# Optimization experiments

Measured on AMD Instinct MI355X. Metric: run time of the kernel, lower is better.

## Reference

```python
import jax, jax.numpy as jnp
import numpy as np

N_NODES = 100000
N_EDGES = 1200000
N_GRAPHS = 2048
NUM_SHAPE, NUM_COLOR, NUM_CLASS = 8, 8, 10
MAX_POS, EMB, HID = 20, 16, 64
IN_DIM = 3 * EMB  # 48


def setup_inputs() -> dict:
    key = jax.random.key(0)
    ks = jax.random.split(key, 14)
    x = jax.random.randint(ks[0], (N_NODES, 3), 0, NUM_SHAPE)
    edge_index = jax.random.randint(ks[1], (2, N_EDGES), 0, N_NODES)
    batch = jnp.sort(jax.random.randint(ks[2], (N_NODES,), 0, N_GRAPHS))
    s = 0.1
    return {
        'x': x, 'edge_index': edge_index, 'batch': batch, 'num_graphs': N_GRAPHS,
        'shape_emb': jax.random.normal(ks[3], (NUM_SHAPE, EMB)) * s,
        'color_emb': jax.random.normal(ks[4], (NUM_COLOR, EMB)) * s,
        'pos_emb': jax.random.normal(ks[5], (MAX_POS, EMB)) * s,
        'W1_l': jax.random.normal(ks[6], (IN_DIM, HID)) * s,
        'W1_r': jax.random.normal(ks[7], (IN_DIM, HID)) * s,
        'b1': jnp.zeros((HID,)),
        'W2_l': jax.random.normal(ks[8], (HID, HID)) * s,
        'W2_r': jax.random.normal(ks[9], (HID, HID)) * s,
        'b2': jnp.zeros((HID,)),
        'Wc': jax.random.normal(ks[10], (HID, NUM_CLASS)) * s,
        'bc': jnp.zeros((NUM_CLASS,)),
    }


def _sage(h, src, dst, W_l, W_r, b, n_nodes):
    # mean-aggregate neighbor features x[src] into dst, then linear combine with root
    agg = jax.ops.segment_sum(h[src], dst, num_segments=n_nodes)
    deg = jax.ops.segment_sum(jnp.ones((src.shape[0],), h.dtype), dst, num_segments=n_nodes)
    mean = agg / jnp.maximum(deg, 1.0)[:, None]
    return mean @ W_l + h @ W_r + b


def reference(x, edge_index, batch, num_graphs, shape_emb, color_emb, pos_emb,
              W1_l, W1_r, b1, W2_l, W2_r, b2, Wc, bc):
    n_nodes = x.shape[0]
    shp = shape_emb[x[:, 0]]
    col = color_emb[x[:, 1]]
    pos = pos_emb[jnp.clip(x[:, 2], 0, MAX_POS - 1)]
    h = jnp.concatenate([shp, col, pos], axis=-1)  # [N, 48]
    src, dst = edge_index[0], edge_index[1]
    h = jax.nn.relu(_sage(h, src, dst, W1_l, W1_r, b1, n_nodes))
    h = jax.nn.relu(_sage(h, src, dst, W2_l, W2_r, b2, n_nodes))
    # global mean pool per graph
    gsum = jax.ops.segment_sum(h, batch, num_segments=num_graphs)
    gcnt = jax.ops.segment_sum(jnp.ones((n_nodes,), h.dtype), batch, num_segments=num_graphs)
    hg = gsum / jnp.maximum(gcnt, 1.0)[:, None]
    return hg @ Wc + bc
```

## Files before the change

kernel.cpp:

```cpp
#include <hip/hip_runtime.h>

#define N_NODES 100000
#define N_EDGES 1200000
#define N_GRAPHS 2048
#define CAPA 16
#define CAPB 32
#define NBUCK 500
#define DPB 200
#define BCAP 4864
#define TILE 4096

typedef unsigned int uint;
typedef unsigned short ushort;
typedef __attribute__((ext_vector_type(8))) short short8;
typedef __attribute__((ext_vector_type(4))) float f32x4;

__device__ __forceinline__ int atomAddI(int* p, int v) {
    return __hip_atomic_fetch_add(p, v, __ATOMIC_RELAXED, __HIP_MEMORY_SCOPE_AGENT);
}
__device__ __forceinline__ int clampPos(int v) { return min(max(v, 0), 19); }
__device__ __forceinline__ uint f2bf(float f) {
    uint b = __float_as_uint(f);
    return (b + 0x7fffu + ((b >> 16) & 1u)) >> 16;
}
__device__ __forceinline__ float bfLo(uint v) { return __uint_as_float(v << 16); }
__device__ __forceinline__ float bfHi(uint v) { return __uint_as_float(v & 0xffff0000u); }
__device__ __forceinline__ int bucketOf(int d) {
    return (int)(((uint)((d >> 3) * 5243)) >> 17);
}

__global__ __launch_bounds__(256) void k_init(
    const int* __restrict__ x,
    const float* __restrict__ se, const float* __restrict__ ce,
    const float* __restrict__ pe,
    const float* __restrict__ W1l, const float* __restrict__ W1r,
    const float* __restrict__ b1,
    const float* __restrict__ W2l, const float* __restrict__ W2r,
    ushort* __restrict__ WLt, ushort* __restrict__ WstkT,
    int* __restrict__ gcur, int* __restrict__ xpk) {
    int t = blockIdx.x * 256 + threadIdx.x;
    if (t < 64 * 96) {
        int col = t / 96, k = t - (t / 96) * 96;
        float v = 0.f;
        if (k < 72) {
            int bkt = (k < 36) ? k : (k - 36);
            const float* erow; int f0;
            if (bkt < 8)       { erow = se + bkt * 16;        f0 = 0;  }
            else if (bkt < 16) { erow = ce + (bkt - 8) * 16;  f0 = 16; }
            else               { erow = pe + (bkt - 16) * 16; f0 = 32; }
            const float* W = (k < 36) ? W1l : W1r;
            float a = 0.f;
            #pragma unroll
            for (int f = 0; f < 16; ++f) a = fmaf(erow[f], W[(f0 + f) * 64 + col], a);
            v = a;
        } else if (k == 72) {
            v = b1[col];
        }
        WLt[t] = (ushort)f2bf(v);
    }
    if (t < 64 * 128) {
        int col = t >> 7, k = t & 127;
        float wv = (k < 64) ? W2r[k * 64 + col] : W2l[(k - 64) * 64 + col];
        WstkT[col * 128 + k] = (ushort)f2bf(wv);
    }
    if (t < NBUCK) gcur[t] = 0;
    for (int i = t; i < N_NODES; i += 256 * 256) {
        int xs = x[i * 3 + 0], xc = x[i * 3 + 1], xp = clampPos(x[i * 3 + 2]);
        xpk[i] = xs | (xc << 8) | (xp << 16);
    }
}

__global__ __launch_bounds__(256) void k_bin(const int* __restrict__ ei,
                                             int* __restrict__ gcur,
                                             int* __restrict__ binned) {
    __shared__ int hist[NBUCK], offs[NBUCK], runc[NBUCK], gbase[NBUCK];
    __shared__ int    stag[TILE];
    __shared__ ushort sbuk[TILE];
    int tid = threadIdx.x;
    int tile_base = blockIdx.x * TILE;
    int tile_n = min(TILE, N_EDGES - tile_base);
    int n4 = tile_n >> 2;
    const int4* s4p = (const int4*)(ei + tile_base);
    const int4* d4p = (const int4*)(ei + N_EDGES + tile_base);

    for (int t = tid; t < NBUCK; t += 256) hist[t] = 0;
    __syncthreads();
    for (int k = tid; k < n4; k += 256) {
        int4 d4 = d4p[k];
        #pragma unroll
        for (int i = 0; i < 4; ++i) atomicAdd(&hist[bucketOf((&d4.x)[i])], 1);
    }
    __syncthreads();
    if (tid < 64) {
        int carry = 0;
        for (int c = 0; c < 8; ++c) {
            int idx = c * 64 + tid;
            int v = (idx < NBUCK) ? hist[idx] : 0;
            int orig = v;
            #pragma unroll
            for (int o = 1; o < 64; o <<= 1) {
                int u = __shfl_up(v, o);
                if (tid >= o) v += u;
            }
            if (idx < NBUCK) offs[idx] = carry + v - orig;
            carry += __shfl(v, 63);
        }
    }
    __syncthreads();
    for (int t = tid; t < NBUCK; t += 256) runc[t] = offs[t];
    __syncthreads();
    for (int k = tid; k < n4; k += 256) {
        int4 d4 = d4p[k];
        int4 s4 = s4p[k];
        #pragma unroll
        for (int i = 0; i < 4; ++i) {
            int d = (&d4.x)[i];
            int b = bucketOf(d);
            int pos = atomicAdd(&runc[b], 1);
            stag[pos] = (&s4.x)[i] | ((d - b * DPB) << 17);
            sbuk[pos] = (ushort)b;
        }
    }
    __syncthreads();
    for (int t = tid; t < NBUCK; t += 256) gbase[t] = atomAddI(&gcur[t], hist[t]);
    __syncthreads();
    for (int i = tid; i < tile_n; i += 256) {
        int b = sbuk[i];
        int o = gbase[b] + (i - offs[b]);
        if (o < BCAP) binned[(size_t)b * BCAP + o] = stag[i];
    }
}

__global__ __launch_bounds__(256) void k_place(const int* __restrict__ binned,
                                               const int* __restrict__ gcur,
                                               int* __restrict__ cursor,
                                               int* __restrict__ slabA,
                                               int* __restrict__ slabB) {
    __shared__ int lslab[DPB][CAPA + CAPB];
    __shared__ int lcur[DPB];
    int b = blockIdx.x;
    int tid = threadIdx.x;
    if (tid < DPB) lcur[tid] = 0;
    __syncthreads();
    int n = min(gcur[b], BCAP);
    const int* in = binned + (size_t)b * BCAP;
    for (int i = tid; i < n; i += 256) {
        int v = in[i];
        int local = v >> 17;
        int slot = atomicAdd(&lcur[local], 1);
        if (slot < CAPA + CAPB) lslab[local][slot] = v & 0x1ffff;
    }
    __syncthreads();
    for (int i = tid; i < DPB * CAPA; i += 256)
        slabA[b * DPB * CAPA + i] = lslab[i >> 4][i & 15];
    for (int i = tid; i < DPB * CAPB; i += 256)
        slabB[b * DPB * CAPB + i] = lslab[i >> 5][CAPA + (i & 31)];
    if (tid < DPB) cursor[b * DPB + tid] = lcur[tid];
}

__device__ __forceinline__ int slabAt(const int* __restrict__ slabA,
                                      const int* __restrict__ slabB,
                                      int row, int idx) {
    return (idx < CAPA) ? slabA[row * CAPA + idx] : slabB[row * CAPB + idx - CAPA];
}

__global__ __launch_bounds__(256) void k_layer1(
    const int* __restrict__ xpk, const int* __restrict__ cursor,
    const int* __restrict__ slabA, const int* __restrict__ slabB,
    const ushort* __restrict__ WLt, uint* __restrict__ AbU) {
    __shared__ int    cnt[16][104];
    __shared__ ushort scnt[16][104];
    __shared__ float  sinv[16];
    __shared__ int    sdeg[16];
    int tid = threadIdx.x;
    int row0 = blockIdx.x * 16;
    for (int i = tid; i < 16 * 104; i += 256) cnt[i / 104][i % 104] = 0;
    if (tid < 16) {
        int dg = cursor[row0 + tid];
        sdeg[tid] = min(dg, CAPA + CAPB);
        sinv[tid] = 1.0f / fmaxf((float)dg, 1.0f);
    }
    __syncthreads();
    for (int i = tid; i < 16 * 48; i += 256) {
        int r = i / 48, idx = i - r * 48;
        if (idx < sdeg[r]) {
            int p = xpk[slabAt(slabA, slabB, row0 + r, idx)];
            atomicAdd(&cnt[r][p & 0xff], 1);
            atomicAdd(&cnt[r][8 + ((p >> 8) & 0xff)], 1);
            atomicAdd(&cnt[r][16 + (p >> 16)], 1);
        }
    }
    if (tid < 16) {
        int p0 = xpk[row0 + tid];
        cnt[tid][36 + (p0 & 0xff)] = 1;
        cnt[tid][44 + ((p0 >> 8) & 0xff)] = 1;
        cnt[tid][52 + (p0 >> 16)] = 1;
        cnt[tid][72] = 1;
    }
    __syncthreads();
    for (int i = tid; i < 16 * 96; i += 256) {
        int r = i / 96, k = i - r * 96;
        float v = (float)cnt[r][k];
        if (k < 36) v *= sinv[r];
        scnt[r][k] = (ushort)f2bf(v);
    }
    __syncthreads();
    int w = tid >> 6, lane = tid & 63;
    int lo16 = lane & 15, hi4 = lane >> 4;
    f32x4 acc = {0.f, 0.f, 0.f, 0.f};
    #pragma unroll
    for (int ks = 0; ks < 3; ++ks) {
        short8 a8 = *(const short8*)(&scnt[lo16][ks * 32 + hi4 * 8]);
        short8 b8 = *(const short8*)(WLt + (w * 16 + lo16) * 96 + ks * 32 + hi4 * 8);
        acc = __builtin_amdgcn_mfma_f32_16x16x32_bf16(a8, b8, acc, 0, 0, 0);
    }
    #pragma unroll
    for (int r = 0; r < 4; ++r) {
        uint rb = f2bf(fmaxf(acc[r], 0.0f));
        uint nxt = __shfl_down(rb, 1);
        if ((lo16 & 1) == 0) {
            int node = row0 + hi4 * 4 + r;
            AbU[(size_t)node * 64 + ((w * 16 + lo16) >> 1)] = rb | (nxt << 16);
        }
    }
}

__global__ __launch_bounds__(256) void k_gather(
    uint* __restrict__ AbU, const int* __restrict__ cursor,
    const int* __restrict__ slabA, const int* __restrict__ slabB) {
    int gid = blockIdx.x * 256 + threadIdx.x;
    int wid = gid >> 6;
    int lane = threadIdx.x & 63;
    int half = lane >> 5, l = lane & 31;
    int row = wid * 2 + half;
    if (row >= N_NODES) return;
    int deg = cursor[row];
    int m = min(deg, CAPA + CAPB);
    int nb0 = (l < m)      ? slabAt(slabA, slabB, row, l)      : 0;
    int nb1 = (l + 32 < m) ? slabB[row * CAPB + l + 32 - CAPA] : 0;
    float ax = 0.f, ay = 0.f;
    int d = 0;
    for (; d + 2 <= m; d += 2) {
        int s0 = __shfl((d < 32) ? nb0 : nb1, (half << 5) | (d & 31));
        int s1 = __shfl((d + 1 < 32) ? nb0 : nb1, (half << 5) | ((d + 1) & 31));
        uint v0 = AbU[(size_t)s0 * 64 + l];
        uint v1 = AbU[(size_t)s1 * 64 + l];
        ax += bfLo(v0) + bfLo(v1);
        ay += bfHi(v0) + bfHi(v1);
    }
    if (d < m) {
        int s = __shfl((d < 32) ? nb0 : nb1, (half << 5) | (d & 31));
        uint v = AbU[(size_t)s * 64 + l];
        ax += bfLo(v);
        ay += bfHi(v);
    }
    float inv = 1.0f / fmaxf((float)deg, 1.0f);
    AbU[(size_t)row * 64 + 32 + l] = f2bf(ax * inv) | (f2bf(ay * inv) << 16);
}

__global__ __launch_bounds__(256) void k_gemm(
    const uint* __restrict__ AbU, const ushort* __restrict__ WstkT,
    const float* __restrict__ b2, uint* __restrict__ h2b) {
    int w = threadIdx.x >> 6, lane = threadIdx.x & 63;
    int lo16 = lane & 15, hi4 = lane >> 4;
    short8 bfr[4][4];
    #pragma unroll
    for (int nb = 0; nb < 4; ++nb) {
        #pragma unroll
        for (int kb = 0; kb < 4; ++kb)
            bfr[nb][kb] = *(const short8*)(WstkT + (nb * 16 + lo16) * 128 + kb * 32 + hi4 * 8);
    }
    float bb[4];
    #pragma unroll
    for (int nb = 0; nb < 4; ++nb) bb[nb] = b2[nb * 16 + lo16];

    int row0 = blockIdx.x * 64 + w * 16;
    int arow = min(row0 + lo16, N_NODES - 1);
    const short8* Arow = (const short8*)(AbU + (size_t)arow * 64);
    short8 a8[4];
    #pragma unroll
    for (int kb = 0; kb < 4; ++kb) a8[kb] = Arow[kb * 4 + hi4];

    f32x4 acc[4] = {{0,0,0,0},{0,0,0,0},{0,0,0,0},{0,0,0,0}};
    #pragma unroll
    for (int kb = 0; kb < 4; ++kb) {
        #pragma unroll
        for (int nb = 0; nb < 4; ++nb)
            acc[nb] = __builtin_amdgcn_mfma_f32_16x16x32_bf16(a8[kb], bfr[nb][kb], acc[nb], 0, 0, 0);
    }
    #pragma unroll
    for (int nb = 0; nb < 4; ++nb) {
        #pragma unroll
        for (int r = 0; r < 4; ++r) {
            uint rb = f2bf(fmaxf(acc[nb][r] + bb[nb], 0.0f));
            uint nxt = __shfl_down(rb, 1);
            if ((lo16 & 1) == 0) {
                int orow = row0 + hi4 * 4 + r;
                if (orow < N_NODES)
                    h2b[(size_t)orow * 32 + ((nb * 16 + lo16) >> 1)] = rb | (nxt << 16);
            }
        }
    }
}

__device__ __forceinline__ int lowerBound(const int* __restrict__ b, int n, int v) {
    int lo = 0, hi = n;
    while (lo < hi) { int mid = (lo + hi) >> 1; if (b[mid] < v) lo = mid + 1; else hi = mid; }
    return lo;
}

__global__ __launch_bounds__(256) void k_pool_final(
    const uint* __restrict__ h2b, const int* __restrict__ batch,
    const float* __restrict__ Wc, const float* __restrict__ bc,
    float* __restrict__ out) {
    int g = blockIdx.x * 8 + (threadIdx.x >> 5);
    if (g >= N_GRAPHS) return;
    int l = threadIdx.x & 31;
    int lo = lowerBound(batch, N_NODES, g);
    int hi = lowerBound(batch, N_NODES, g + 1);
    float ax0 = 0.f, ay0 = 0.f, ax1 = 0.f, ay1 = 0.f;
    int n = lo;
    for (; n + 2 <= hi; n += 2) {
        uint v0 = h2b[(size_t)n * 32 + l];
        uint v1 = h2b[(size_t)(n + 1) * 32 + l];
        ax0 += bfLo(v0); ay0 += bfHi(v0);
        ax1 += bfLo(v1); ay1 += bfHi(v1);
    }
    if (n < hi) {
        uint v = h2b[(size_t)n * 32 + l];
        ax0 += bfLo(v); ay0 += bfHi(v);
    }
    float inv = 1.0f / fmaxf((float)(hi - lo), 1.0f);
    float mx = (ax0 + ax1) * inv, my = (ay0 + ay1) * inv;
    #pragma unroll
    for (int c = 0; c < 10; ++c) {
        float p = fmaf(mx, Wc[(2 * l) * 10 + c], my * Wc[(2 * l + 1) * 10 + c]);
        #pragma unroll
        for (int off = 16; off >= 1; off >>= 1) p += __shfl_xor(p, off);
        if (l == 0) out[g * 10 + c] = p + bc[c];
    }
}

extern "C" void kernel_launch(void* const* d_in, const int* in_sizes, int n_in,
                              void* d_out, int out_size, void* d_ws, size_t ws_size,
                              hipStream_t stream) {
    const int* x     = (const int*)d_in[0];
    const int* ei    = (const int*)d_in[1];
    const int* batch = (const int*)d_in[2];
    const float* se  = (const float*)d_in[4];
    const float* ce  = (const float*)d_in[5];
    const float* pe  = (const float*)d_in[6];
    const float* W1l = (const float*)d_in[7];
    const float* W1r = (const float*)d_in[8];
    const float* b1  = (const float*)d_in[9];
    const float* W2l = (const float*)d_in[10];
    const float* W2r = (const float*)d_in[11];
    const float* b2  = (const float*)d_in[12];
    const float* Wc  = (const float*)d_in[13];
    const float* bc  = (const float*)d_in[14];

    float* ws    = (float*)d_ws;
    uint*  AbU   = (uint*)ws;
    uint*  h2b   = (uint*)(ws + 6400000);
    int*   binned= (int*)ws;
    int*   slabA = (int*)(ws + 12800000);
    int*   slabB = (int*)(ws + 14400000);
    int*   cursor= (int*)(ws + 17600000);
    int*   xpk   = (int*)(ws + 17700000);
    ushort* WstkT= (ushort*)(ws + 17806000);
    ushort* WLt  = (ushort*)(ws + 17810100);
    int*   gcur  = (int*)(ws + 17814000);

    k_init<<<256, 256, 0, stream>>>(x, se, ce, pe, W1l, W1r, b1, W2l, W2r,
                                    WLt, WstkT, gcur, xpk);
    k_bin<<<(N_EDGES + TILE - 1) / TILE, 256, 0, stream>>>(ei, gcur, binned);
    k_place<<<NBUCK, 256, 0, stream>>>(binned, gcur, cursor, slabA, slabB);
    k_layer1<<<N_NODES / 16, 256, 0, stream>>>(xpk, cursor, slabA, slabB, WLt, AbU);
    k_gather<<<12500, 256, 0, stream>>>(AbU, cursor, slabA, slabB);
    k_gemm<<<(N_NODES + 63) / 64, 256, 0, stream>>>(AbU, WstkT, b2, h2b);
    k_pool_final<<<N_GRAPHS / 8, 256, 0, stream>>>(h2b, batch, Wc, bc, (float*)d_out);
}
```

Baseline: 130.4 us.

## Fuse init preprocessing into binning kernel, halve bin tile, widen pooling per graph

Folds the weight-folding, weight transpose and node packing work of the init kernel into the edge-binning kernel as grid-stride loops, and replaces the bucket-counter reset with an async memset. This removes one kernel launch and its serialization. The binning tile shrinks so more blocks run. Pooling now uses a full 64-lane wave per graph, with two halves reading alternate nodes and combining through a shuffle. The memset still costs a queue operation, and the smaller tiles mean more global atomics on the bucket counters.

```diff
diff --git a/kernel.cpp b/kernel.cpp
--- a/kernel.cpp
+++ b/kernel.cpp
@@ -8,7 +8,7 @@
 #define NBUCK 500
 #define DPB 200
 #define BCAP 4864
-#define TILE 4096
+#define TILE 2048
 
 typedef unsigned int uint;
 typedef unsigned short ushort;
@@ -29,7 +29,8 @@
     return (int)(((uint)((d >> 3) * 5243)) >> 17);
 }
 
-__global__ __launch_bounds__(256) void k_init(
+__global__ __launch_bounds__(256) void k_bin(
+    const int* __restrict__ ei,
     const int* __restrict__ x,
     const float* __restrict__ se, const float* __restrict__ ce,
     const float* __restrict__ pe,
@@ -37,10 +38,17 @@
     const float* __restrict__ b1,
     const float* __restrict__ W2l, const float* __restrict__ W2r,
     ushort* __restrict__ WLt, ushort* __restrict__ WstkT,
-    int* __restrict__ gcur, int* __restrict__ xpk) {
-    int t = blockIdx.x * 256 + threadIdx.x;
-    if (t < 64 * 96) {
-        int col = t / 96, k = t - (t / 96) * 96;
+    int* __restrict__ xpk,
+    int* __restrict__ gcur, int* __restrict__ binned) {
+    __shared__ int hist[NBUCK], offs[NBUCK], runc[NBUCK], gbase[NBUCK];
+    __shared__ int    stag[TILE];
+    __shared__ ushort sbuk[TILE];
+    int tid = threadIdx.x;
+    int gt = blockIdx.x * 256 + tid;
+    int gstride = gridDim.x * 256;
+
+    for (int t = gt; t < 64 * 96; t += gstride) {
+        int col = t / 96, k = t - col * 96;
         float v = 0.f;
         if (k < 72) {
             int bkt = (k < 36) ? k : (k - 36);
@@ -58,25 +66,16 @@
         }
         WLt[t] = (ushort)f2bf(v);
     }
-    if (t < 64 * 128) {
+    for (int t = gt; t < 64 * 128; t += gstride) {
         int col = t >> 7, k = t & 127;
         float wv = (k < 64) ? W2r[k * 64 + col] : W2l[(k - 64) * 64 + col];
         WstkT[col * 128 + k] = (ushort)f2bf(wv);
     }
-    if (t < NBUCK) gcur[t] = 0;
-    for (int i = t; i < N_NODES; i += 256 * 256) {
+    for (int i = gt; i < N_NODES; i += gstride) {
         int xs = x[i * 3 + 0], xc = x[i * 3 + 1], xp = clampPos(x[i * 3 + 2]);
         xpk[i] = xs | (xc << 8) | (xp << 16);
     }
-}
-
-__global__ __launch_bounds__(256) void k_bin(const int* __restrict__ ei,
-                                             int* __restrict__ gcur,
-                                             int* __restrict__ binned) {
-    __shared__ int hist[NBUCK], offs[NBUCK], runc[NBUCK], gbase[NBUCK];
-    __shared__ int    stag[TILE];
-    __shared__ ushort sbuk[TILE];
-    int tid = threadIdx.x;
+
     int tile_base = blockIdx.x * TILE;
     int tile_n = min(TILE, N_EDGES - tile_base);
     int n4 = tile_n >> 2;
@@ -313,31 +312,39 @@
     const uint* __restrict__ h2b, const int* __restrict__ batch,
     const float* __restrict__ Wc, const float* __restrict__ bc,
     float* __restrict__ out) {
-    int g = blockIdx.x * 8 + (threadIdx.x >> 5);
+    int g = blockIdx.x * 4 + (threadIdx.x >> 6);
     if (g >= N_GRAPHS) return;
-    int l = threadIdx.x & 31;
+    int lane = threadIdx.x & 63;
+    int half = lane >> 5, l = lane & 31;
     int lo = lowerBound(batch, N_NODES, g);
     int hi = lowerBound(batch, N_NODES, g + 1);
     float ax0 = 0.f, ay0 = 0.f, ax1 = 0.f, ay1 = 0.f;
     int n = lo;
-    for (; n + 2 <= hi; n += 2) {
-        uint v0 = h2b[(size_t)n * 32 + l];
-        uint v1 = h2b[(size_t)(n + 1) * 32 + l];
+    for (; n + 4 <= hi; n += 4) {
+        uint v0 = h2b[(size_t)(n + half) * 32 + l];
+        uint v1 = h2b[(size_t)(n + 2 + half) * 32 + l];
         ax0 += bfLo(v0); ay0 += bfHi(v0);
         ax1 += bfLo(v1); ay1 += bfHi(v1);
     }
-    if (n < hi) {
+    for (; n + 2 <= hi; n += 2) {
+        uint v = h2b[(size_t)(n + half) * 32 + l];
+        ax0 += bfLo(v); ay0 += bfHi(v);
+    }
+    if (n < hi && half == 0) {
         uint v = h2b[(size_t)n * 32 + l];
         ax0 += bfLo(v); ay0 += bfHi(v);
     }
+    float ax = ax0 + ax1, ay = ay0 + ay1;
+    ax += __shfl_down(ax, 32);
+    ay += __shfl_down(ay, 32);
     float inv = 1.0f / fmaxf((float)(hi - lo), 1.0f);
-    float mx = (ax0 + ax1) * inv, my = (ay0 + ay1) * inv;
+    float mx = ax * inv, my = ay * inv;
     #pragma unroll
     for (int c = 0; c < 10; ++c) {
         float p = fmaf(mx, Wc[(2 * l) * 10 + c], my * Wc[(2 * l + 1) * 10 + c]);
         #pragma unroll
         for (int off = 16; off >= 1; off >>= 1) p += __shfl_xor(p, off);
-        if (l == 0) out[g * 10 + c] = p + bc[c];
+        if (lane == 0) out[g * 10 + c] = p + bc[c];
     }
 }
 
@@ -371,12 +378,12 @@
     ushort* WLt  = (ushort*)(ws + 17810100);
     int*   gcur  = (int*)(ws + 17814000);
 
-    k_init<<<256, 256, 0, stream>>>(x, se, ce, pe, W1l, W1r, b1, W2l, W2r,
-                                    WLt, WstkT, gcur, xpk);
-    k_bin<<<(N_EDGES + TILE - 1) / TILE, 256, 0, stream>>>(ei, gcur, binned);
+    hipMemsetAsync(gcur, 0, NBUCK * 4, stream);
+    k_bin<<<(N_EDGES + TILE - 1) / TILE, 256, 0, stream>>>(
+        ei, x, se, ce, pe, W1l, W1r, b1, W2l, W2r, WLt, WstkT, xpk, gcur, binned);
     k_place<<<NBUCK, 256, 0, stream>>>(binned, gcur, cursor, slabA, slabB);
     k_layer1<<<N_NODES / 16, 256, 0, stream>>>(xpk, cursor, slabA, slabB, WLt, AbU);
     k_gather<<<12500, 256, 0, stream>>>(AbU, cursor, slabA, slabB);
     k_gemm<<<(N_NODES + 63) / 64, 256, 0, stream>>>(AbU, WstkT, b2, h2b);
-    k_pool_final<<<N_GRAPHS / 8, 256, 0, stream>>>(h2b, batch, Wc, bc, (float*)d_out);
-}
+    k_pool_final<<<(N_GRAPHS + 3) / 4, 256, 0, stream>>>(h2b, batch, Wc, bc, (float*)d_out);
+}
```

Measured after the change: 130.8 us. About the same (+0.3%).
